# Optimization experiments

Hardware: AMD Instinct MI355X
Metric: run time of the kernel (lower is better)

Reference implementation:

```python
import jax, jax.numpy as jnp
import numpy as np

EMBED_DIM = 1024
NUM_HEADS = 16
HEAD_DIM = EMBED_DIM // NUM_HEADS


def setup_inputs() -> dict:
    key = jax.random.key(0)
    kx, kw1, kb1, kw2, kb2 = jax.random.split(key, 5)
    D = EMBED_DIM
    # torch nn.Linear default init: U(-1/sqrt(in), 1/sqrt(in)); use scaled uniform
    lim = 1.0 / np.sqrt(D)
    return {
        "x": jax.random.normal(kx, (2, 2048, D), dtype=jnp.float32),
        "w_qkv": jax.random.uniform(kw1, (D, 3 * D), jnp.float32, -lim, lim),
        "b_qkv": jax.random.uniform(kb1, (3 * D,), jnp.float32, -lim, lim),
        "w_o": jax.random.uniform(kw2, (D, D), jnp.float32, -lim, lim),
        "b_o": jax.random.uniform(kb2, (D,), jnp.float32, -lim, lim),
    }


def reference(x, w_qkv, b_qkv, w_o, b_o):
    B, S, D = x.shape
    H, hd = NUM_HEADS, HEAD_DIM
    qkv = x @ w_qkv + b_qkv                       # [B,S,3D]
    qkv = qkv.reshape(B, S, H, 3, hd)             # per-head [q|k|v] blocks of size hd
    q = qkv[:, :, :, 0].transpose(0, 2, 1, 3)     # [B,H,S,hd]
    k = qkv[:, :, :, 1].transpose(0, 2, 1, 3)
    v = qkv[:, :, :, 2].transpose(0, 2, 1, 3)
    scale = hd ** -0.5
    scores = jnp.einsum('bhqd,bhkd->bhqk', q, k) * scale
    attn = jax.nn.softmax(scores, axis=-1)
    out = jnp.einsum('bhqk,bhkd->bhqd', attn, v)  # [B,H,S,hd]
    out = out.transpose(0, 2, 1, 3).reshape(B, S, D)
    return out @ w_o + b_o
```

## Files before the change

### kernel.cpp

```cpp
#include <hip/hip_runtime.h>

typedef __attribute__((ext_vector_type(8))) _Float16 half8;
typedef __attribute__((ext_vector_type(4))) _Float16 half4;
typedef __attribute__((ext_vector_type(4))) float f32x4;
typedef __attribute__((ext_vector_type(16))) float f32x16;
typedef __attribute__((ext_vector_type(4))) int i32x4;

typedef __attribute__((address_space(1))) void* gptr_t;
typedef __attribute__((address_space(3))) void* lptr_t;
#define GLL16(g, l) __builtin_amdgcn_global_load_lds((gptr_t)(g), (lptr_t)(l), 16, 0, 0)

__device__ __forceinline__ float fast_exp2(float x) {
  float r;
  asm volatile("v_exp_f32 %0, %1" : "=v"(r) : "v"(x));
  return r;
}


__global__ void cvt_x_kernel(const float* __restrict__ x, _Float16* __restrict__ xh) {
  size_t i = (size_t)blockIdx.x * blockDim.x + threadIdx.x;
  float4 v = *reinterpret_cast<const float4*>(x + i * 4);
  half4 o = { (_Float16)v.x, (_Float16)v.y, (_Float16)v.z, (_Float16)v.w };
  *reinterpret_cast<half4*>(xh + i * 4) = o;
}

__global__ void transpose_cvt_kernel(const float* __restrict__ w, _Float16* __restrict__ wt, int N) {
  __shared__ _Float16 lds[64][72];
  const int t = threadIdx.x;
  const int n0 = blockIdx.x * 64, k0 = blockIdx.y * 64;
#pragma unroll
  for (int rep = 0; rep < 4; ++rep) {
    int k = rep * 16 + (t >> 4);
    int nc = (t & 15) * 4;
    float4 v = *reinterpret_cast<const float4*>(&w[(size_t)(k0 + k) * N + n0 + nc]);
    lds[nc + 0][k] = (_Float16)v.x;
    lds[nc + 1][k] = (_Float16)v.y;
    lds[nc + 2][k] = (_Float16)v.z;
    lds[nc + 3][k] = (_Float16)v.w;
  }
  __syncthreads();
#pragma unroll
  for (int rep = 0; rep < 2; ++rep) {
    int ch = rep * 256 + t;
    int n = ch >> 3, kc = ch & 7;
    half8 o = *reinterpret_cast<const half8*>(&lds[n][kc * 8]);
    *reinterpret_cast<half8*>(&wt[(size_t)(n0 + n) * 1024 + k0 + kc * 8]) = o;
  }
}


__global__ __launch_bounds__(256, 2)
void gemm_qkv(const _Float16* __restrict__ A, const _Float16* __restrict__ Bt,
              const float* __restrict__ bias,
              _Float16* __restrict__ qh, _Float16* __restrict__ kh,
              _Float16* __restrict__ vT) {
  __shared__ __align__(16) _Float16 Ah[128 * 64];
  __shared__ __align__(16) _Float16 Bh[128 * 64];
  const int t = threadIdx.x;
  const int w = t >> 6, ln = t & 63, G = ln >> 4, c = ln & 15;
  const int m0 = blockIdx.y * 128, n0 = blockIdx.x * 128;
  const int wr = w >> 1, wc = w & 1;
  f32x4 acc[4][4] = {};
  for (int kt = 0; kt < 1024; kt += 64) {
#pragma unroll
    for (int i = 0; i < 4; ++i) {
      int ch = i * 256 + t;
      int row = ch >> 3, kc = ch & 7;
      int kk = kt + ((kc ^ (row & 7)) << 3);
      int ldsbase = (i * 256 + w * 64) * 8;
      GLL16(A + (size_t)(m0 + row) * 1024 + kk, Ah + ldsbase);
      GLL16(Bt + (size_t)(n0 + row) * 1024 + kk, Bh + ldsbase);
    }
    __syncthreads();
    half8 aF[2][4], bF[2][4];
#pragma unroll
    for (int ks = 0; ks < 2; ++ks)
#pragma unroll
      for (int i = 0; i < 4; ++i) {
        int ra = wr * 64 + i * 16 + c;
        aF[ks][i] = *reinterpret_cast<const half8*>(&Ah[ra * 64 + (((ks * 4 + G) ^ (ra & 7)) << 3)]);
        int rb = wc * 64 + i * 16 + c;
        bF[ks][i] = *reinterpret_cast<const half8*>(&Bh[rb * 64 + (((ks * 4 + G) ^ (rb & 7)) << 3)]);
      }
#pragma unroll
    for (int ks = 0; ks < 2; ++ks)
#pragma unroll
      for (int mi = 0; mi < 4; ++mi)
#pragma unroll
        for (int ni = 0; ni < 4; ++ni)
          acc[mi][ni] = __builtin_amdgcn_mfma_f32_16x16x32_f16(aF[ks][mi], bF[ks][ni], acc[mi][ni], 0, 0, 0);
    __syncthreads();
  }
  const int mbase = m0 + wr * 64, nbase = n0 + wc * 64;
  const int Gp = ((G & 1) << 1) | (G >> 1);
#pragma unroll
  for (int ni = 0; ni < 4; ++ni) {
    int n = nbase + ni * 16 + c;
    float bv = bias[n];
    int h = n / 192;
    int rem = n - h * 192;
    int tt = rem >> 6, d = rem & 63;
#pragma unroll
    for (int mi = 0; mi < 4; ++mi) {
      if (tt == 2) {
        int mb = mbase + mi * 16;
        int bb = mb >> 11, s0 = mb & 2047;
        size_t bh = (size_t)(bb * 16 + h);
        half4 o = { (_Float16)(acc[mi][ni][0] + bv), (_Float16)(acc[mi][ni][1] + bv),
                    (_Float16)(acc[mi][ni][2] + bv), (_Float16)(acc[mi][ni][3] + bv) };
        *reinterpret_cast<half4*>(&vT[(bh * 64 + d) * 2048 + s0 + 4 * Gp]) = o;
      } else {
#pragma unroll
        for (int r = 0; r < 4; ++r) {
          int m = mbase + mi * 16 + 4 * G + r;
          int bb = m >> 11, s = m & 2047;
          float val = acc[mi][ni][r] + bv;
          size_t bh = (size_t)(bb * 16 + h);
          if (tt == 0) qh[(bh * 2048 + s) * 64 + d] = (_Float16)(val * (0.125f * 1.44269504089f));
          else         kh[(bh * 2048 + s) * 64 + d] = (_Float16)val;
        }
      }
    }
  }
}


__global__ __launch_bounds__(256, 2)
void gemm_o(const _Float16* __restrict__ A, const _Float16* __restrict__ Bt,
            const float* __restrict__ bias, float* __restrict__ outf) {
  __shared__ __align__(16) _Float16 Ah[128 * 64];
  __shared__ __align__(16) _Float16 Bh[64 * 64];
  const int t = threadIdx.x;
  const int w = t >> 6, ln = t & 63, G = ln >> 4, c = ln & 15;
  const int m0 = blockIdx.y * 128, n0 = blockIdx.x * 64;
  const int wr = w >> 1, wc = w & 1;
  f32x4 acc[4][2] = {};
  for (int kt = 0; kt < 1024; kt += 64) {
#pragma unroll
    for (int i = 0; i < 4; ++i) {
      int ch = i * 256 + t;
      int row = ch >> 3, kc = ch & 7;
      int kk = kt + ((kc ^ (row & 7)) << 3);
      GLL16(A + (size_t)(m0 + row) * 1024 + kk, Ah + (i * 256 + w * 64) * 8);
    }
#pragma unroll
    for (int i = 0; i < 2; ++i) {
      int ch = i * 256 + t;
      int row = ch >> 3, kc = ch & 7;
      int kk = kt + ((kc ^ (row & 7)) << 3);
      GLL16(Bt + (size_t)(n0 + row) * 1024 + kk, Bh + (i * 256 + w * 64) * 8);
    }
    __syncthreads();
    half8 aF[2][4], bF[2][2];
#pragma unroll
    for (int ks = 0; ks < 2; ++ks) {
#pragma unroll
      for (int i = 0; i < 4; ++i) {
        int ra = wr * 64 + i * 16 + c;
        aF[ks][i] = *reinterpret_cast<const half8*>(&Ah[ra * 64 + (((ks * 4 + G) ^ (ra & 7)) << 3)]);
      }
#pragma unroll
      for (int i = 0; i < 2; ++i) {
        int rb = wc * 32 + i * 16 + c;
        bF[ks][i] = *reinterpret_cast<const half8*>(&Bh[rb * 64 + (((ks * 4 + G) ^ (rb & 7)) << 3)]);
      }
    }
#pragma unroll
    for (int ks = 0; ks < 2; ++ks)
#pragma unroll
      for (int mi = 0; mi < 4; ++mi)
#pragma unroll
        for (int ni = 0; ni < 2; ++ni)
          acc[mi][ni] = __builtin_amdgcn_mfma_f32_16x16x32_f16(aF[ks][mi], bF[ks][ni], acc[mi][ni], 0, 0, 0);
    __syncthreads();
  }
  const int mbase = m0 + wr * 64, nbase = n0 + wc * 32;
#pragma unroll
  for (int ni = 0; ni < 2; ++ni) {
    int n = nbase + ni * 16 + c;
    float bv = bias[n];
#pragma unroll
    for (int mi = 0; mi < 4; ++mi)
#pragma unroll
      for (int r = 0; r < 4; ++r) {
        int m = mbase + mi * 16 + 4 * G + r;
        outf[(size_t)m * 1024 + n] = acc[mi][ni][r] + bv;
      }
  }
}


__global__ __launch_bounds__(256, 2)
void attn_kernel(const _Float16* __restrict__ qh, const _Float16* __restrict__ kh,
                 const _Float16* __restrict__ vT, _Float16* __restrict__ ao) {
  __shared__ __align__(16) _Float16 Kt[3][64 * 64];
  __shared__ __align__(16) _Float16 Vt[4][64 * 64];
  const int t = threadIdx.x;
  const int w = t >> 6, ln = t & 63, lo = ln & 31, hi = ln >> 5;
  const int bid = blockIdx.x;
  const int xcd = bid & 7, tt = bid >> 3;
  const int bh = xcd * 4 + (tt >> 4);
  const int qb = tt & 15;
  const int q0 = qb * 128 + w * 32;
  const _Float16* qp = qh + (size_t)bh * 2048 * 64;
  const _Float16* kp = kh + (size_t)bh * 2048 * 64;
  const _Float16* vp = vT + (size_t)bh * 64 * 2048;

  half8 qf[4];
#pragma unroll
  for (int sl = 0; sl < 4; ++sl)
    qf[sl] = *reinterpret_cast<const half8*>(qp + (size_t)(q0 + lo) * 64 + sl * 16 + hi * 8);

  f32x16 O0 = {}, O1 = {};
  float plsum = 0.f;
  unsigned pk[4][4];

  auto stage = [&](int kb, int vb, int jt) {
#pragma unroll
    for (int i = 0; i < 2; ++i) {
      int ch = i * 256 + t;
      int row = ch >> 3, cc = ch & 7;
      int sw = ((cc ^ ((row ^ (row >> 3)) & 7)) << 3);
      int ldsbase = (i * 256 + w * 64) * 8;
      GLL16(kp + (size_t)(jt + row) * 64 + sw, &Kt[kb][ldsbase]);
      GLL16(vp + (size_t)row * 2048 + jt + sw, &Vt[vb][ldsbase]);
    }
  };

  auto qkt = [&](int kb, f32x16& s0, f32x16& s1) {
    __builtin_amdgcn_s_setprio(1);
#pragma unroll
    for (int sl = 0; sl < 4; ++sl) {
      const int ch = sl * 2 + hi;
      const int r0 = lo, r1 = 32 + lo;
      half8 k0 = *reinterpret_cast<const half8*>(&Kt[kb][r0 * 64 + ((ch ^ ((r0 ^ (r0 >> 3)) & 7)) << 3)]);
      s0 = __builtin_amdgcn_mfma_f32_32x32x16_f16(k0, qf[sl], s0, 0, 0, 0);
      half8 k1 = *reinterpret_cast<const half8*>(&Kt[kb][r1 * 64 + ((ch ^ ((r1 ^ (r1 >> 3)) & 7)) << 3)]);
      s1 = __builtin_amdgcn_mfma_f32_32x32x16_f16(k1, qf[sl], s1, 0, 0, 0);
    }
    __builtin_amdgcn_s_setprio(0);
  };

  auto pv = [&](int vb) {
    __builtin_amdgcn_s_setprio(1);
#pragma unroll
    for (int kb2 = 0; kb2 < 4; ++kb2) {
      i32x4 pi = { (int)pk[kb2][0], (int)pk[kb2][1], (int)pk[kb2][2], (int)pk[kb2][3] };
      half8 pf = __builtin_bit_cast(half8, pi);
      const int ch = kb2 * 2 + hi;
      const int r0 = lo, r1 = 32 + lo;
      half8 v0 = *reinterpret_cast<const half8*>(&Vt[vb][r0 * 64 + ((ch ^ ((r0 ^ (r0 >> 3)) & 7)) << 3)]);
      O0 = __builtin_amdgcn_mfma_f32_32x32x16_f16(v0, pf, O0, 0, 0, 0);
      half8 v1 = *reinterpret_cast<const half8*>(&Vt[vb][r1 * 64 + ((ch ^ ((r1 ^ (r1 >> 3)) & 7)) << 3)]);
      O1 = __builtin_amdgcn_mfma_f32_32x32x16_f16(v1, pf, O1, 0, 0, 0);
    }
    __builtin_amdgcn_s_setprio(0);
  };

  auto smpack = [&](f32x16& s0, f32x16& s1) {
#pragma unroll
    for (int i = 0; i < 16; ++i) s0[i] = fast_exp2(s0[i]);
#pragma unroll
    for (int i = 0; i < 16; ++i) s1[i] = fast_exp2(s1[i]);
    float sm[8];
#pragma unroll
    for (int i = 0; i < 8; ++i) sm[i] = (s0[i] + s0[i + 8]) + (s1[i] + s1[i + 8]);
#pragma unroll
    for (int i = 0; i < 4; ++i) sm[i] += sm[i + 4];
    plsum += (sm[0] + sm[1]) + (sm[2] + sm[3]);
#pragma unroll
    for (int kh2 = 0; kh2 < 2; ++kh2)
#pragma unroll
      for (int j = 0; j < 4; ++j) {
        pk[kh2][j]     = __builtin_bit_cast(unsigned, __builtin_amdgcn_cvt_pkrtz(s0[kh2 * 8 + 2 * j], s0[kh2 * 8 + 2 * j + 1]));
        pk[2 + kh2][j] = __builtin_bit_cast(unsigned, __builtin_amdgcn_cvt_pkrtz(s1[kh2 * 8 + 2 * j], s1[kh2 * 8 + 2 * j + 1]));
      }
  };

  stage(0, 0, 0);
  stage(1, 1, 64);
  stage(2, 2, 128);
  asm volatile("s_waitcnt vmcnt(8)" ::: "memory");
  __builtin_amdgcn_s_barrier();
  {
    f32x16 s0 = {}, s1 = {};
    qkt(0, s0, s1);
    smpack(s0, s1);
  }
  asm volatile("s_waitcnt vmcnt(4)" ::: "memory");
  __builtin_amdgcn_s_barrier();

  for (int it = 0; it < 31; ++it) {
    if (it < 29) {
      int T = it + 3;
      stage(T % 3, T & 3, T * 64);
    }
    f32x16 s0 = {}, s1 = {};
    qkt((it + 1) % 3, s0, s1);
    pv(it & 3);
    smpack(s0, s1);
    if (it < 29) asm volatile("s_waitcnt vmcnt(4)" ::: "memory");
    else         asm volatile("s_waitcnt vmcnt(0)" ::: "memory");
    __builtin_amdgcn_s_barrier();
  }
  pv(31 & 3);

  float lsum = plsum + __shfl_xor(plsum, 32);
  float inv = 1.f / lsum;
  const int bb = bh >> 4, hd_i = bh & 15;
  const size_t srow = (size_t)bb * 2048 + q0 + lo;
  _Float16* aob = ao + srow * 1024 + hd_i * 64 + hi * 4;
#pragma unroll
  for (int rq = 0; rq < 4; ++rq) {
    half4 o0 = { (_Float16)(O0[4 * rq] * inv), (_Float16)(O0[4 * rq + 1] * inv),
                 (_Float16)(O0[4 * rq + 2] * inv), (_Float16)(O0[4 * rq + 3] * inv) };
    *reinterpret_cast<half4*>(aob + rq * 8) = o0;
    half4 o1 = { (_Float16)(O1[4 * rq] * inv), (_Float16)(O1[4 * rq + 1] * inv),
                 (_Float16)(O1[4 * rq + 2] * inv), (_Float16)(O1[4 * rq + 3] * inv) };
    *reinterpret_cast<half4*>(aob + 32 + rq * 8) = o1;
  }
}


extern "C" void kernel_launch(void* const* d_in, const int* in_sizes, int n_in,
                              void* d_out, int out_size, void* d_ws, size_t ws_size,
                              hipStream_t stream) {
  const float* x     = (const float*)d_in[0];
  const float* w_qkv = (const float*)d_in[1];
  const float* b_qkv = (const float*)d_in[2];
  const float* w_o   = (const float*)d_in[3];
  const float* b_o   = (const float*)d_in[4];
  float* out = (float*)d_out;
  char* ws = (char*)d_ws;
  _Float16* xh    = (_Float16*)(ws);
  _Float16* wqkvT = (_Float16*)(ws + ((size_t)8  << 20));
  _Float16* woT   = (_Float16*)(ws + ((size_t)14 << 20));
  _Float16* qh    = (_Float16*)(ws + ((size_t)16 << 20));
  _Float16* kh    = (_Float16*)(ws + ((size_t)24 << 20));
  _Float16* vT    = (_Float16*)(ws + ((size_t)32 << 20));
  _Float16* ao    = (_Float16*)(ws + ((size_t)40 << 20));

  cvt_x_kernel<<<4096, 256, 0, stream>>>(x, xh);
  transpose_cvt_kernel<<<dim3(48, 16), 256, 0, stream>>>(w_qkv, wqkvT, 3072);
  transpose_cvt_kernel<<<dim3(16, 16), 256, 0, stream>>>(w_o, woT, 1024);
  gemm_qkv<<<dim3(24, 32), 256, 0, stream>>>(xh, wqkvT, b_qkv, qh, kh, vT);
  attn_kernel<<<512, 256, 0, stream>>>(qh, kh, vT, ao);
  gemm_o<<<dim3(16, 32), 256, 0, stream>>>(ao, woT, b_o, out);
}
```

Measured before the change: 119.6 us.

## Deepen attention software pipeline to two-stage QK lookahead and merge prep kernels

The attention loop now computes QK^T two tiles ahead using ping-pong score registers, with a five-deep V ring buffer, so the exp/pack of one tile overlaps the MFMAs of the next and the PV of an earlier one. The priority hints now cover the combined QK+PV MFMA section instead of each part separately. The three preprocessing kernels (x conversion and the two weight transposes) are fused into a single launch to cut launch overhead. This adds register pressure from the extra score accumulators and about 8KB more LDS, which could reduce occupancy under launch_bounds(256,2).

Measured after the change: 183.5 us. +53.4%, slower.

```diff
diff --git a/kernel.cpp b/kernel.cpp
--- a/kernel.cpp
+++ b/kernel.cpp
@@ -17,17 +17,23 @@
 }
 
 
-__global__ void cvt_x_kernel(const float* __restrict__ x, _Float16* __restrict__ xh) {
-  size_t i = (size_t)blockIdx.x * blockDim.x + threadIdx.x;
-  float4 v = *reinterpret_cast<const float4*>(x + i * 4);
-  half4 o = { (_Float16)v.x, (_Float16)v.y, (_Float16)v.z, (_Float16)v.w };
-  *reinterpret_cast<half4*>(xh + i * 4) = o;
-}
-
-__global__ void transpose_cvt_kernel(const float* __restrict__ w, _Float16* __restrict__ wt, int N) {
+__global__ void prep_kernel(const float* __restrict__ x, _Float16* __restrict__ xh,
+                            const float* __restrict__ w_qkv, _Float16* __restrict__ wqkvT,
+                            const float* __restrict__ w_o, _Float16* __restrict__ woT) {
   __shared__ _Float16 lds[64][72];
+  const int bid = blockIdx.x;
   const int t = threadIdx.x;
-  const int n0 = blockIdx.x * 64, k0 = blockIdx.y * 64;
+  if (bid < 4096) {
+    size_t i = (size_t)bid * 256 + t;
+    float4 v = *reinterpret_cast<const float4*>(x + i * 4);
+    half4 o = { (_Float16)v.x, (_Float16)v.y, (_Float16)v.z, (_Float16)v.w };
+    *reinterpret_cast<half4*>(xh + i * 4) = o;
+    return;
+  }
+  const float* w; _Float16* wt; int N, bx, by;
+  if (bid < 4096 + 768) { int b = bid - 4096; w = w_qkv; wt = wqkvT; N = 3072; bx = b % 48; by = b / 48; }
+  else                  { int b = bid - 4864; w = w_o;   wt = woT;   N = 1024; bx = b & 15; by = b >> 4; }
+  const int n0 = bx * 64, k0 = by * 64;
 #pragma unroll
   for (int rep = 0; rep < 4; ++rep) {
     int k = rep * 16 + (t >> 4);
@@ -194,7 +200,7 @@
 void attn_kernel(const _Float16* __restrict__ qh, const _Float16* __restrict__ kh,
                  const _Float16* __restrict__ vT, _Float16* __restrict__ ao) {
   __shared__ __align__(16) _Float16 Kt[3][64 * 64];
-  __shared__ __align__(16) _Float16 Vt[4][64 * 64];
+  __shared__ __align__(16) _Float16 Vt[5][64 * 64];
   const int t = threadIdx.x;
   const int w = t >> 6, ln = t & 63, lo = ln & 31, hi = ln >> 5;
   const int bid = blockIdx.x;
@@ -228,21 +234,20 @@
   };
 
   auto qkt = [&](int kb, f32x16& s0, f32x16& s1) {
-    __builtin_amdgcn_s_setprio(1);
+    f32x16 a = {}, b = {};
 #pragma unroll
     for (int sl = 0; sl < 4; ++sl) {
       const int ch = sl * 2 + hi;
       const int r0 = lo, r1 = 32 + lo;
       half8 k0 = *reinterpret_cast<const half8*>(&Kt[kb][r0 * 64 + ((ch ^ ((r0 ^ (r0 >> 3)) & 7)) << 3)]);
-      s0 = __builtin_amdgcn_mfma_f32_32x32x16_f16(k0, qf[sl], s0, 0, 0, 0);
+      a = __builtin_amdgcn_mfma_f32_32x32x16_f16(k0, qf[sl], a, 0, 0, 0);
       half8 k1 = *reinterpret_cast<const half8*>(&Kt[kb][r1 * 64 + ((ch ^ ((r1 ^ (r1 >> 3)) & 7)) << 3)]);
-      s1 = __builtin_amdgcn_mfma_f32_32x32x16_f16(k1, qf[sl], s1, 0, 0, 0);
-    }
-    __builtin_amdgcn_s_setprio(0);
+      b = __builtin_amdgcn_mfma_f32_32x32x16_f16(k1, qf[sl], b, 0, 0, 0);
+    }
+    s0 = a; s1 = b;
   };
 
   auto pv = [&](int vb) {
-    __builtin_amdgcn_s_setprio(1);
 #pragma unroll
     for (int kb2 = 0; kb2 < 4; ++kb2) {
       i32x4 pi = { (int)pk[kb2][0], (int)pk[kb2][1], (int)pk[kb2][2], (int)pk[kb2][3] };
@@ -254,7 +259,6 @@
       half8 v1 = *reinterpret_cast<const half8*>(&Vt[vb][r1 * 64 + ((ch ^ ((r1 ^ (r1 >> 3)) & 7)) << 3)]);
       O1 = __builtin_amdgcn_mfma_f32_32x32x16_f16(v1, pf, O1, 0, 0, 0);
     }
-    __builtin_amdgcn_s_setprio(0);
   };
 
   auto smpack = [&](f32x16& s0, f32x16& s1) {
@@ -276,34 +280,65 @@
         pk[2 + kh2][j] = __builtin_bit_cast(unsigned, __builtin_amdgcn_cvt_pkrtz(s1[kh2 * 8 + 2 * j], s1[kh2 * 8 + 2 * j + 1]));
       }
   };
+
+  f32x16 sA0, sA1, sB0, sB1;
 
   stage(0, 0, 0);
   stage(1, 1, 64);
   stage(2, 2, 128);
   asm volatile("s_waitcnt vmcnt(8)" ::: "memory");
   __builtin_amdgcn_s_barrier();
-  {
-    f32x16 s0 = {}, s1 = {};
-    qkt(0, s0, s1);
-    smpack(s0, s1);
-  }
+  qkt(0, sA0, sA1);
   asm volatile("s_waitcnt vmcnt(4)" ::: "memory");
   __builtin_amdgcn_s_barrier();
 
-  for (int it = 0; it < 31; ++it) {
-    if (it < 29) {
-      int T = it + 3;
-      stage(T % 3, T & 3, T * 64);
-    }
-    f32x16 s0 = {}, s1 = {};
-    qkt((it + 1) % 3, s0, s1);
-    pv(it & 3);
-    smpack(s0, s1);
-    if (it < 29) asm volatile("s_waitcnt vmcnt(4)" ::: "memory");
-    else         asm volatile("s_waitcnt vmcnt(0)" ::: "memory");
-    __builtin_amdgcn_s_barrier();
-  }
-  pv(31 & 3);
+  stage(0, 3, 192);
+  __builtin_amdgcn_s_setprio(1);
+  qkt(1, sB0, sB1);
+  __builtin_amdgcn_s_setprio(0);
+  smpack(sA0, sA1);
+  asm volatile("s_waitcnt vmcnt(4)" ::: "memory");
+  __builtin_amdgcn_s_barrier();
+
+  for (int base = 1; base <= 27; base += 2) {
+    {
+      int T = base + 3;
+      stage(T % 3, T % 5, T * 64);
+      __builtin_amdgcn_s_setprio(1);
+      qkt((base + 1) % 3, sA0, sA1);
+      pv((base - 1) % 5);
+      __builtin_amdgcn_s_setprio(0);
+      smpack(sB0, sB1);
+      asm volatile("s_waitcnt vmcnt(4)" ::: "memory");
+      __builtin_amdgcn_s_barrier();
+    }
+    {
+      int T = base + 4;
+      stage(T % 3, T % 5, T * 64);
+      __builtin_amdgcn_s_setprio(1);
+      qkt((base + 2) % 3, sB0, sB1);
+      pv(base % 5);
+      __builtin_amdgcn_s_setprio(0);
+      smpack(sA0, sA1);
+      asm volatile("s_waitcnt vmcnt(4)" ::: "memory");
+      __builtin_amdgcn_s_barrier();
+    }
+  }
+  __builtin_amdgcn_s_setprio(1);
+  qkt(30 % 3, sA0, sA1);
+  pv(28 % 5);
+  __builtin_amdgcn_s_setprio(0);
+  smpack(sB0, sB1);
+  asm volatile("s_waitcnt vmcnt(0)" ::: "memory");
+  __builtin_amdgcn_s_barrier();
+  __builtin_amdgcn_s_setprio(1);
+  qkt(31 % 3, sB0, sB1);
+  pv(29 % 5);
+  __builtin_amdgcn_s_setprio(0);
+  smpack(sA0, sA1);
+  pv(30 % 5);
+  smpack(sB0, sB1);
+  pv(31 % 5);
 
   float lsum = plsum + __shfl_xor(plsum, 32);
   float inv = 1.f / lsum;
@@ -340,9 +375,7 @@
   _Float16* vT    = (_Float16*)(ws + ((size_t)32 << 20));
   _Float16* ao    = (_Float16*)(ws + ((size_t)40 << 20));
 
-  cvt_x_kernel<<<4096, 256, 0, stream>>>(x, xh);
-  transpose_cvt_kernel<<<dim3(48, 16), 256, 0, stream>>>(w_qkv, wqkvT, 3072);
-  transpose_cvt_kernel<<<dim3(16, 16), 256, 0, stream>>>(w_o, woT, 1024);
+  prep_kernel<<<5120, 256, 0, stream>>>(x, xh, w_qkv, wqkvT, w_o, woT);
   gemm_qkv<<<dim3(24, 32), 256, 0, stream>>>(xh, wqkvT, b_qkv, qh, kh, vT);
   attn_kernel<<<512, 256, 0, stream>>>(qh, kh, vT, ao);
   gemm_o<<<dim3(16, 32), 256, 0, stream>>>(ao, woT, b_o, out);
```
